# Kernel tuning notes

Measured on AMD Instinct MI355X. Metric: run time of the kernel, lower is better.

Reference implementation:

```python
import jax, jax.numpy as jnp
from jax import lax
import numpy as np

B, S, PRE = 64, 12, 12
N04, N07, N08 = 307, 883, 170
IN_DIM, HID, ENC = 128, 256, 256


def setup_inputs() -> dict:
    key = jax.random.key(0)
    ks = iter(jax.random.split(key, 64))
    nrm = lambda shape, s=1.0: jax.random.normal(next(ks), shape, jnp.float32) * s
    uni = lambda shape: jax.random.uniform(next(ks), shape, jnp.float32)
    d = {
        "vec_pems04": nrm((N04, IN_DIM)),
        "vec_pems07": nrm((N07, IN_DIM)),
        "vec_pems08": nrm((N08, IN_DIM)),
        "feat": nrm((B, S, N04)),
        "adj_pems04": uni((N04, N04)),
        "adj_pems07": uni((N07, N07)),
        "adj_pems08": uni((N08, N08)),
    }
    for p in ("ex4", "ex7", "ex8"):
        d[p + "_W1"] = nrm((IN_DIM, HID), 0.05)
        d[p + "_b1"] = jnp.zeros((HID,), jnp.float32)
        d[p + "_W2"] = nrm((HID, ENC), 0.05)
        d[p + "_b2"] = jnp.zeros((ENC,), jnp.float32)
        d[p + "_g"] = jnp.ones((ENC,), jnp.float32)
        d[p + "_bt"] = jnp.zeros((ENC,), jnp.float32)
        d[p + "_eps"] = jnp.ones((1,), jnp.float32)
    d["gru_W1"] = nrm((HID + 1, 2 * HID), 0.05)
    d["gru_b1"] = jnp.ones((2 * HID,), jnp.float32)  # VGRULinear bias=1.0
    d["gru_W2"] = nrm((HID + 1, HID), 0.05)
    d["gru_b2"] = jnp.zeros((HID,), jnp.float32)
    d["feat_W"] = nrm((ENC, ENC), 0.05)
    d["feat_b"] = jnp.zeros((1,), jnp.float32)
    d["lin_W"] = nrm((HID + ENC, HID), 0.05)
    d["lin_b"] = jnp.zeros((HID,), jnp.float32)
    d["out_W"] = nrm((HID, PRE), 0.05)
    d["out_b"] = jnp.zeros((PRE,), jnp.float32)
    d["eval_flag"] = 0
    return d


def _extract(vec, adj, W1, b1, W2, b2, g, bt, eps1):
    # Extractor_N2V with etype='gin', BatchNorm1d in training mode (batch stats)
    h = vec @ W1 + b1
    pooled = adj @ h
    deg = adj @ jnp.ones((adj.shape[0], 1), adj.dtype)
    h = pooled / deg + eps1 * h
    mu = jnp.mean(h, axis=0)
    var = jnp.mean(jnp.square(h - mu), axis=0)  # biased var, as torch BN
    h = (h - mu) * lax.rsqrt(var + 1e-5) * g + bt
    return h @ W2 + b2


def _predict(feat, node_feat, gru_W1, gru_b1, gru_W2, gru_b2, feat_W, feat_b, lin_W, lin_b):
    Bb, Ss, N = feat.shape
    H = gru_W2.shape[1]
    E = node_feat.shape[-1]
    # feat @ weights + bias is timestep-invariant -> hoist out of the scan (same math)
    fp = jnp.broadcast_to(node_feat[None], (Bb, N, E)).reshape(Bb * N, E) @ feat_W + feat_b

    def vl(x, hs, W, b):
        # VGRULinear: concat scalar input with per-node hidden, flatten per node
        cat = jnp.concatenate([x[..., None], hs.reshape(Bb, N, H)], axis=2).reshape(Bb * N, H + 1)
        return (cat @ W + b).reshape(Bb, -1)

    def step(h, x):
        gates = jax.nn.sigmoid(vl(x, h, gru_W1, gru_b1))  # (B, N*2H)
        r, u = jnp.split(gates, 2, axis=1)                # chunk on flat dim, as in source
        c = jnp.tanh(vl(x, r * h, gru_W2, gru_b2))
        nh = u * h + (1.0 - u) * c
        nh = jnp.concatenate([nh.reshape(Bb * N, H), fp], axis=1) @ lin_W + lin_b
        nh = nh.reshape(Bb, N * H)
        return nh, None

    h0 = jnp.zeros((Bb, N * H), feat.dtype)
    hT, _ = lax.scan(step, h0, jnp.swapaxes(feat, 0, 1))  # scan over seq_len
    return hT.reshape(Bb * N, H)  # last output


def reference(vec_pems04, vec_pems07, vec_pems08, feat, adj_pems04, adj_pems07, adj_pems08,
              ex4_W1, ex4_b1, ex4_W2, ex4_b2, ex4_g, ex4_bt, ex4_eps,
              ex7_W1, ex7_b1, ex7_W2, ex7_b2, ex7_g, ex7_bt, ex7_eps,
              ex8_W1, ex8_b1, ex8_W2, ex8_b2, ex8_g, ex8_bt, ex8_eps,
              gru_W1, gru_b1, gru_W2, gru_b2, feat_W, feat_b, lin_W, lin_b,
              out_W, out_b, eval_flag):
    # dataset='4' != ft_dataset='8', eval=False branch
    f4 = _extract(vec_pems04, adj_pems04, ex4_W1, ex4_b1, ex4_W2, ex4_b2, ex4_g, ex4_bt, ex4_eps)
    f7 = _extract(vec_pems07, adj_pems07, ex7_W1, ex7_b1, ex7_W2, ex7_b2, ex7_g, ex7_bt, ex7_eps)
    f8 = _extract(vec_pems08, adj_pems08, ex8_W1, ex8_b1, ex8_W2, ex8_b2, ex8_g, ex8_bt, ex8_eps)
    last = _predict(feat, f4, gru_W1, gru_b1, gru_W2, gru_b2, feat_W, feat_b, lin_W, lin_b)
    pred = (last @ out_W + out_b).reshape(feat.shape[0], adj_pems04.shape[0], -1)
    return pred, f4, f7, f8
```

## Files before the change

kernel.cpp:

```cpp
#include <hip/hip_runtime.h>
#include <hip/hip_bf16.h>
#include <math.h>

using bf16 = __hip_bfloat16;
using short8  = __attribute__((ext_vector_type(8))) short;
using float4v = __attribute__((ext_vector_type(4))) float;

#define B_   64
#define S_   12
#define N04  307
#define N07  883
#define N08  170
#define BN   (B_ * N04)
#define HID  256
#define ENC  256
#define PRE  12
#define UOFF (N04 * HID)

constexpr int c_Mi[3]   = {N04, N07, N08};
constexpr int c_Kp[3]   = {320, 896, 192};
constexpr int c_Moff[3] = {0, N04, N04 + N07};
constexpr int c_Aoff[3] = {0, N04 * 320, N04 * 320 + N07 * 896};
constexpr int c_Cb[3]   = {0, 320, 320 + 896};
#define MTOT  (N04 + N07 + N08)
#define H0T_LD 1408

#define NT 38
constexpr int g_sz[NT] = {
    39296, 113024, 21760, 235776, 94249, 779689, 28900,
    32768, 256, 65536, 256, 256, 256, 1,
    32768, 256, 65536, 256, 256, 256, 1,
    32768, 256, 65536, 256, 256, 256, 1,
    131584, 512, 65792, 256, 65536, 1, 131072, 256, 3072, 12
};
struct Tables { int off[NT + 1]; int blk[NT + 1]; };
constexpr Tables mk_tables() {
    Tables t{};
    t.off[0] = 0; t.blk[0] = 0;
    for (int i = 0; i < NT; ++i) {
        t.off[i + 1] = t.off[i] + g_sz[i];
        t.blk[i + 1] = t.blk[i] + (g_sz[i] + 1023) / 1024;
    }
    return t;
}
constexpr Tables g_tbl = mk_tables();

static __device__ __forceinline__ float fsigmoid(float t) {
    return __builtin_amdgcn_rcpf(1.f + __expf(-t));
}
static __device__ __forceinline__ float ftanh(float t) {
    return 1.f - 2.f * __builtin_amdgcn_rcpf(__expf(2.f * t) + 1.f);
}

static __device__ __forceinline__ void bsplit(int m, int& b, int& nn) {
    b  = (int)(((unsigned long long)(unsigned)m * 27980243ull) >> 33);
    nn = m - b * N04;
}

__global__ void sniff_kernel(const unsigned short* raw, int* flag)
{
    __shared__ int sh[256];
    int t = threadIdx.x, cnt = 0;
    for (int i = t; i < 2048; i += 256) {
        unsigned int w = ((unsigned int)raw[i]) << 16;
        float a = fabsf(__uint_as_float(w));
        if (a > 1e-3f && a < 100.f) cnt++;
    }
    sh[t] = cnt; __syncthreads();
    for (int off = 128; off > 0; off >>= 1) {
        if (t < off) sh[t] += sh[t + off];
        __syncthreads();
    }
    if (t == 0) *flag = (sh[0] > 1536) ? 1 : 0;
}

struct Ptrs { const void* p[NT]; };

__global__ __launch_bounds__(256) void convert_all(Ptrs a, float* arena, const int* flag)
{
    const int bf = *flag;
    int b = blockIdx.x;
    int t = 0;
    while (b >= g_tbl.blk[t + 1]) ++t;
    const int base = (b - g_tbl.blk[t]) * 1024;
    const int n = g_sz[t];
    const void* src = a.p[t];
    float* dst = arena + g_tbl.off[t];
#pragma unroll
    for (int k = 0; k < 4; ++k) {
        int j = base + k * 256 + threadIdx.x;
        if (j < n)
            dst[j] = bf ? __bfloat162float(((const bf16*)src)[j]) : ((const float*)src)[j];
    }
}

__global__ __launch_bounds__(256) void prep_weights(const float* w1, const float* w2, const float* wl,
                                                    bf16* WgT, bf16* WcT, bf16* WlT)
{
    int id = blockIdx.x * 256 + threadIdx.x;
    if (id < 131072) {
        int n = id >> 8, k = id & 255;
        WgT[id] = __float2bfloat16(w1[(size_t)(1 + k) * 512 + n]);
    } else if (id < 196608) {
        int r = id - 131072; int n = r >> 8, k = r & 255;
        WcT[r] = __float2bfloat16(w2[(size_t)(1 + k) * 256 + n]);
    } else if (id < 262144) {
        int r = id - 196608; int n = r >> 8, k = r & 255;
        WlT[r] = __float2bfloat16(wl[(size_t)k * 256 + n]);
    }
}

__global__ __launch_bounds__(256) void prep_adjB(const float* a4, const float* a7, const float* a8, bf16* adjB)
{
    int z = blockIdx.z;
    int Mi = c_Mi[z], Kp = c_Kp[z];
    int m = blockIdx.x;
    if (m >= Mi) return;
    const float* src = (z == 0) ? a4 : (z == 1) ? a7 : a8;
    bf16* dst = adjB + c_Aoff[z] + (size_t)m * Kp;
    for (int c = threadIdx.x; c < Kp; c += 256)
        dst[c] = (c < Mi) ? __float2bfloat16(src[(size_t)m * Mi + c]) : __float2bfloat16(0.f);
}

__global__ __launch_bounds__(256) void prep_transposes(
    const float* v4, const float* v7, const float* v8,
    const float* w1a, const float* w1b, const float* w1c,
    const float* w2a, const float* w2b, const float* w2c,
    const float* featW, const float* linW, const float* outW,
    bf16* vecB, bf16* W1T, bf16* W2T, bf16* featWT, bf16* linW2T, bf16* outWT)
{
    int id = blockIdx.x * 256 + threadIdx.x;
    if (id < 174080) {
        int r = id >> 7, c = id & 127;
        float v = (r < N04) ? v4[(size_t)r * 128 + c]
                : (r < N04 + N07) ? v7[(size_t)(r - N04) * 128 + c]
                : v8[(size_t)(r - N04 - N07) * 128 + c];
        vecB[id] = __float2bfloat16(v);
    } else if (id < 174080 + 98304) {
        int r = id - 174080; int z = r >> 15; int rem = r & 32767;
        int n = rem >> 7, k = rem & 127;
        const float* w = (z == 0) ? w1a : (z == 1) ? w1b : w1c;
        W1T[r] = __float2bfloat16(w[(size_t)k * 256 + n]);
    } else if (id < 272384 + 196608) {
        int r = id - 272384; int z = r >> 16; int rem = r & 65535;
        int n = rem >> 8, k = rem & 255;
        const float* w = (z == 0) ? w2a : (z == 1) ? w2b : w2c;
        W2T[r] = __float2bfloat16(w[(size_t)k * 256 + n]);
    } else if (id < 468992 + 65536) {
        int r = id - 468992; int n = r >> 8, k = r & 255;
        featWT[r] = __float2bfloat16(featW[(size_t)k * 256 + n]);
    } else if (id < 534528 + 65536) {
        int r = id - 534528; int n = r >> 8, k = r & 255;
        linW2T[r] = __float2bfloat16(linW[(size_t)(256 + k) * 256 + n]);
    } else if (id < 600064 + 16384) {
        int r = id - 600064; int p = r >> 8, k = r & 255;
        outWT[r] = __float2bfloat16((p < PRE) ? outW[(size_t)k * PRE + p] : 0.f);
    }
}
#define PREP_T_TOT (600064 + 16384)

struct GemmZ {
    const unsigned short* A[3];
    const unsigned short* BT[3];
    int M[3]; int K[3]; int lda[3]; int ldb[3];
};

template <typename EP>
__global__ __launch_bounds__(256) void gemm_mfma64(GemmZ p, int Nv, EP ep)
{
    const int z = blockIdx.z;
    const int gx = gridDim.x, gy = gridDim.y;
    const int nwg = gx * gy;
    const int flat = blockIdx.y * gx + blockIdx.x;
    const int xcd = flat & 7, lin = flat >> 3;
    const int q = nwg >> 3, r = nwg & 7;
    const int wg = (xcd < r ? xcd * (q + 1) : r * (q + 1) + (xcd - r) * q) + lin;
    const int bx = wg / gy;
    const int by = wg - bx * gy;

    const int M = p.M[z], K = p.K[z], lda = p.lda[z], ldb = p.ldb[z];
    const int m0 = bx * 64;
    const int n0 = by * 64;
    if (m0 >= M) return;
    __shared__ __align__(16) unsigned short As[64 * 72];
    __shared__ __align__(16) unsigned short Bs[64 * 72];
    const int t = threadIdx.x;
    const int srow  = t >> 2;
    const int skoff = (t & 3) * 16;
    const int lane = t & 63;
    const int w  = t >> 6;
    const int wm = (w & 1) * 32;
    const int wn = (w >> 1) * 32;
    const int l15 = lane & 15;
    const int l4  = lane >> 4;

    float4v acc[2][2];
#pragma unroll
    for (int i = 0; i < 2; ++i)
#pragma unroll
        for (int j = 0; j < 2; ++j) acc[i][j] = (float4v)(0.f);

    const int gm = m0 + srow;
    const bool avalid = (gm < M);
    const unsigned short* aptr = p.A[z]  + (size_t)gm * lda + skoff;
    const unsigned short* bptr = p.BT[z] + (size_t)(n0 + srow) * ldb + skoff;
    unsigned short* asw = &As[srow * 72 + skoff];
    unsigned short* bsw = &Bs[srow * 72 + skoff];
    const uint4 z4 = {0, 0, 0, 0};

    for (int kt = 0; kt < K; kt += 64) {
        uint4 av0 = avalid ? *(const uint4*)(aptr + kt)     : z4;
        uint4 av1 = avalid ? *(const uint4*)(aptr + kt + 8) : z4;
        uint4 bv0 = *(const uint4*)(bptr + kt);
        uint4 bv1 = *(const uint4*)(bptr + kt + 8);
        __syncthreads();
        *(uint4*)(asw)     = av0;
        *(uint4*)(asw + 8) = av1;
        *(uint4*)(bsw)     = bv0;
        *(uint4*)(bsw + 8) = bv1;
        __syncthreads();
#pragma unroll
        for (int ks = 0; ks < 2; ++ks) {
            short8 af[2], bq[2];
#pragma unroll
            for (int mi = 0; mi < 2; ++mi)
                af[mi] = *(const short8*)&As[(wm + mi * 16 + l15) * 72 + ks * 32 + l4 * 8];
#pragma unroll
            for (int ni = 0; ni < 2; ++ni)
                bq[ni] = *(const short8*)&Bs[(wn + ni * 16 + l15) * 72 + ks * 32 + l4 * 8];
#pragma unroll
            for (int mi = 0; mi < 2; ++mi)
#pragma unroll
                for (int ni = 0; ni < 2; ++ni)
                    acc[mi][ni] = __builtin_amdgcn_mfma_f32_16x16x32_bf16(af[mi], bq[ni], acc[mi][ni], 0, 0, 0);
        }
    }
#pragma unroll
    for (int mi = 0; mi < 2; ++mi) {
#pragma unroll
        for (int r2 = 0; r2 < 4; ++r2) {
            int m = m0 + wm + mi * 16 + l4 * 4 + r2;
            if (m >= M) continue;
#pragma unroll
            for (int ni = 0; ni < 2; ++ni) {
                int n = n0 + wn + ni * 16 + l15;
                if (n < Nv) ep(z, m, n, acc[mi][ni][r2]);
            }
        }
    }
}

struct EPg1 {
    const float* b1[3]; float* h0F; bf16* h0T;
    __device__ void operator()(int z, int m, int n, float v) const {
        v += b1[z][n];
        int gr = c_Moff[z] + m;
        h0F[(size_t)gr * 256 + n] = v;
        h0T[(size_t)n * H0T_LD + c_Cb[z] + m] = __float2bfloat16(v);
    }
};
struct EPg2 {
    const float* deg; const float* h0F; float* h1F; const float* eps[3];
    __device__ void operator()(int z, int m, int n, float v) const {
        int gr = c_Moff[z] + m;
        h1F[(size_t)gr * 256 + n] = v / deg[gr] + eps[z][0] * h0F[(size_t)gr * 256 + n];
    }
};
struct EPg3 {
    const float* b2[3]; void* outbase; size_t ooff[3]; const int* flag; bf16* f4B;
    __device__ void operator()(int z, int m, int n, float v) const {
        v += b2[z][n];
        size_t i = ooff[z] + (size_t)m * 256 + n;
        if (*flag) ((bf16*)outbase)[i] = __float2bfloat16(v);
        else       ((float*)outbase)[i] = v;
        if (z == 0) f4B[(size_t)m * 256 + n] = __float2bfloat16(v);
    }
};
struct EPfp2a {
    const float* sb; bf16* fpreB;
    __device__ void operator()(int z, int m, int n, float v) const {
        fpreB[(size_t)m * 256 + n] = __float2bfloat16(v + sb[0]);
    }
};
struct EPfp2b {
    float* fp2;
    __device__ void operator()(int z, int m, int n, float v) const {
        fp2[(size_t)m * 256 + n] = v;
    }
};
struct EPpred {
    const float* ob; void* outbase; const int* flag;
    __device__ void operator()(int z, int m, int n, float v) const {
        v += ob[n];
        size_t i = (size_t)m * PRE + n;
        if (*flag) ((bf16*)outbase)[i] = __float2bfloat16(v);
        else       ((float*)outbase)[i] = v;
    }
};

struct EPgates3 {
    bf16* rh; bf16* ub; const bf16* hB;
    const float* b1; const float* w1r0; const float* feat; int s;
    __device__ void operator()(int z, int m, int n, float v) const {
        int b, nn; bsplit(m, b, nn);
        float x = feat[((size_t)b * S_ + s) * N04 + nn];
        float g = fsigmoid(v + b1[n] + x * w1r0[n]);
        int p = nn * 512 + n;
        int base = b * UOFF;
        if (p < UOFF) {
            int idx = base + p;
            rh[idx] = __float2bfloat16(g * __bfloat162float(hB[idx]));
        } else {
            ub[base + (p - UOFF)] = __float2bfloat16(g);
        }
    }
};
struct EPcand3 {
    bf16* uhc; const bf16* ub; const bf16* hB;
    const float* b2; const float* w2r0; const float* feat; int s;
    __device__ void operator()(int z, int m, int n, float v) const {
        int b, nn; bsplit(m, b, nn);
        float x = feat[((size_t)b * S_ + s) * N04 + nn];
        float c = ftanh(v + b2[n] + x * w2r0[n]);
        size_t idx = (size_t)m * 256 + n;
        float u = __bfloat162float(ub[idx]);
        float h = __bfloat162float(hB[idx]);
        uhc[idx] = __float2bfloat16(u * h + (1.f - u) * c);
    }
};
struct EPlin3 {
    bf16* hB; const float* lb; const float* fp2;
    __device__ void operator()(int z, int m, int n, float v) const {
        int b, nn; bsplit(m, b, nn);
        hB[(size_t)m * 256 + n] = __float2bfloat16(v + lb[n] + fp2[(size_t)nn * 256 + n]);
    }
};

__global__ __launch_bounds__(256) void init_step0(const float* feat,
                                                  const float* b1, const float* w1r0,
                                                  const float* b2, const float* w2r0,
                                                  bf16* uhc)
{
    int m = blockIdx.x, n = threadIdx.x;
    int b, nn; bsplit(m, b, nn);
    const float* fb = feat + (size_t)b * S_ * N04;
    float c = ftanh(b2[n] + fb[nn] * w2r0[n]);
    int p = UOFF + nn * 256 + n;
    int gn = p >> 9, gc = p & 511;
    float u = fsigmoid(b1[gc] + fb[gn] * w1r0[gc]);
    uhc[(size_t)m * 256 + n] = __float2bfloat16((1.f - u) * c);
}

__global__ void deg_all(const float* a4, const float* a7, const float* a8, float* deg)
{
    int z = blockIdx.z;
    int Mi = c_Mi[z];
    int row = blockIdx.x;
    if (row >= Mi) return;
    const float* adj = (z == 0) ? a4 : (z == 1) ? a7 : a8;
    float s = 0.f;
    for (int j = threadIdx.x; j < Mi; j += 64) s += adj[(size_t)row * Mi + j];
#pragma unroll
    for (int off = 32; off > 0; off >>= 1) s += __shfl_down(s, off, 64);
    if (threadIdx.x == 0) deg[c_Moff[z] + row] = s;
}

__global__ __launch_bounds__(256) void stats_all(const float* h1F, float* mu, float* rstd)
{
    int z = blockIdx.z;
    int Mi = c_Mi[z], moff = c_Moff[z];
    int j = blockIdx.x;
    int t = threadIdx.x;
    float s = 0.f, ss = 0.f;
    for (int i = t; i < Mi; i += 256) {
        float v = h1F[(size_t)(moff + i) * 256 + j];
        s += v; ss += v * v;
    }
    __shared__ float sh[256], sh2[256];
    sh[t] = s; sh2[t] = ss;
    __syncthreads();
    for (int off = 128; off > 0; off >>= 1) {
        if (t < off) { sh[t] += sh[t + off]; sh2[t] += sh2[t + off]; }
        __syncthreads();
    }
    if (t == 0) {
        float m = sh[0] / (float)Mi;
        float var = sh2[0] / (float)Mi - m * m;
        mu[z * 256 + j] = m;
        rstd[z * 256 + j] = rsqrtf(var + 1e-5f);
    }
}

__global__ __launch_bounds__(256) void norm_all(const float* h1F, const float* mu, const float* rstd,
                                                const float* ga, const float* gb, const float* gc,
                                                const float* ba, const float* bb, const float* bc,
                                                bf16* nh1B)
{
    int r = blockIdx.x;
    int n = threadIdx.x;
    int z = (r < N04) ? 0 : (r < N04 + N07) ? 1 : 2;
    const float* g  = (z == 0) ? ga : (z == 1) ? gb : gc;
    const float* bt = (z == 0) ? ba : (z == 1) ? bb : bc;
    float v = (h1F[(size_t)r * 256 + n] - mu[z * 256 + n]) * rstd[z * 256 + n] * g[n] + bt[n];
    nh1B[(size_t)r * 256 + n] = __float2bfloat16(v);
}

extern "C" void kernel_launch(void* const* d_in, const int* in_sizes, int n_in,
                              void* d_out, int out_size, void* d_ws, size_t ws_size,
                              hipStream_t stream)
{
    char* wp = (char*)d_ws;
    auto carve = [&](size_t bytes) -> void* {
        void* p = (void*)wp;
        wp += (bytes + 255) & ~(size_t)255;
        return p;
    };
    float* arena = (float*)carve((size_t)g_tbl.off[NT] * 4);
    int*   flag  = (int*)carve(256);
    bf16*  hb_a  = (bf16*)carve((size_t)BN * HID * 2);
    bf16*  hb_b  = (bf16*)carve((size_t)BN * HID * 2);
    bf16*  rh    = (bf16*)carve((size_t)BN * HID * 2);
    bf16*  uhc   = (bf16*)carve((size_t)BN * HID * 2);
    bf16*  ubufB = (bf16*)carve((size_t)BN * HID * 2);
    bf16*  WgT   = (bf16*)carve((size_t)512 * 256 * 2);
    bf16*  WcT   = (bf16*)carve((size_t)256 * 256 * 2);
    bf16*  WlT   = (bf16*)carve((size_t)256 * 256 * 2);
    bf16*  vecB  = (bf16*)carve((size_t)MTOT * 128 * 2);
    bf16*  adjB  = (bf16*)carve((size_t)(N04 * 320 + N07 * 896 + N08 * 192) * 2);
    bf16*  W1T   = (bf16*)carve((size_t)3 * 256 * 128 * 2);
    bf16*  W2T   = (bf16*)carve((size_t)3 * 256 * 256 * 2);
    bf16*  featWT= (bf16*)carve((size_t)256 * 256 * 2);
    bf16*  linW2T= (bf16*)carve((size_t)256 * 256 * 2);
    bf16*  outWT = (bf16*)carve((size_t)64 * 256 * 2);
    float* h0F   = (float*)carve((size_t)MTOT * 256 * 4);
    bf16*  h0T   = (bf16*)carve((size_t)256 * H0T_LD * 2);
    float* h1F   = (float*)carve((size_t)MTOT * 256 * 4);
    bf16*  nh1B  = (bf16*)carve((size_t)MTOT * 256 * 2);
    float* degb  = (float*)carve((size_t)MTOT * 4);
    float* mub   = (float*)carve(3 * 256 * 4);
    float* rstdb = (float*)carve(3 * 256 * 4);
    bf16*  f4B   = (bf16*)carve((size_t)N04 * 256 * 2);
    bf16*  fpreB = (bf16*)carve((size_t)N04 * 256 * 2);
    float* fp2   = (float*)carve((size_t)N04 * 256 * 4);

    sniff_kernel<<<1, 256, 0, stream>>>((const unsigned short*)d_in[0], flag);
    Ptrs ptrs;
    for (int i = 0; i < NT; ++i) ptrs.p[i] = d_in[i];
    convert_all<<<g_tbl.blk[NT], 256, 0, stream>>>(ptrs, arena, flag);

    auto A = [&](int i) -> const float* { return arena + g_tbl.off[i]; };

    prep_weights<<<1024, 256, 0, stream>>>(A(28), A(30), A(34), WgT, WcT, WlT);
    prep_adjB<<<dim3(N07, 1, 3), 256, 0, stream>>>(A(4), A(5), A(6), adjB);
    prep_transposes<<<(PREP_T_TOT + 255) / 256, 256, 0, stream>>>(
        A(0), A(1), A(2), A(7), A(14), A(21), A(9), A(16), A(23),
        A(32), A(34), A(36), vecB, W1T, W2T, featWT, linW2T, outWT);

    hipMemsetAsync(h0T, 0, (size_t)256 * H0T_LD * 2, stream);

    const size_t o_f4 = (size_t)B_ * N04 * PRE;
    const size_t o_f7 = o_f4 + (size_t)N04 * ENC;
    const size_t o_f8 = o_f7 + (size_t)N07 * ENC;

    deg_all<<<dim3(N07, 1, 3), 64, 0, stream>>>(A(4), A(5), A(6), degb);

    {
        GemmZ p;
        for (int z = 0; z < 3; ++z) {
            p.A[z] = (const unsigned short*)(vecB + (size_t)c_Moff[z] * 128);
            p.BT[z] = (const unsigned short*)(W1T + (size_t)z * 256 * 128);
            p.M[z] = c_Mi[z]; p.K[z] = 128; p.lda[z] = 128; p.ldb[z] = 128;
        }
        EPg1 ep{{A(8), A(15), A(22)}, h0F, h0T};
        gemm_mfma64<<<dim3(14, 4, 3), 256, 0, stream>>>(p, 256, ep);
    }
    {
        GemmZ p;
        for (int z = 0; z < 3; ++z) {
            p.A[z] = (const unsigned short*)(adjB + c_Aoff[z]);
            p.BT[z] = (const unsigned short*)(h0T + c_Cb[z]);
            p.M[z] = c_Mi[z]; p.K[z] = c_Kp[z]; p.lda[z] = c_Kp[z]; p.ldb[z] = H0T_LD;
        }
        EPg2 ep{degb, h0F, h1F, {A(13), A(20), A(27)}};
        gemm_mfma64<<<dim3(14, 4, 3), 256, 0, stream>>>(p, 256, ep);
    }
    stats_all<<<dim3(256, 1, 3), 256, 0, stream>>>(h1F, mub, rstdb);
    norm_all<<<MTOT, 256, 0, stream>>>(h1F, mub, rstdb, A(11), A(18), A(25), A(12), A(19), A(26), nh1B);
    {
        GemmZ p;
        for (int z = 0; z < 3; ++z) {
            p.A[z] = (const unsigned short*)(nh1B + (size_t)c_Moff[z] * 256);
            p.BT[z] = (const unsigned short*)(W2T + (size_t)z * 256 * 256);
            p.M[z] = c_Mi[z]; p.K[z] = 256; p.lda[z] = 256; p.ldb[z] = 256;
        }
        EPg3 ep{{A(10), A(17), A(24)}, d_out, {o_f4, o_f7, o_f8}, flag, f4B};
        gemm_mfma64<<<dim3(14, 4, 3), 256, 0, stream>>>(p, 256, ep);
    }
    {
        GemmZ p{};
        p.A[0] = (const unsigned short*)f4B; p.BT[0] = (const unsigned short*)featWT;
        p.M[0] = N04; p.K[0] = 256; p.lda[0] = 256; p.ldb[0] = 256;
        gemm_mfma64<<<dim3(5, 4, 1), 256, 0, stream>>>(p, 256, EPfp2a{A(33), fpreB});
        p.A[0] = (const unsigned short*)fpreB; p.BT[0] = (const unsigned short*)linW2T;
        gemm_mfma64<<<dim3(5, 4, 1), 256, 0, stream>>>(p, 256, EPfp2b{fp2});
    }

    const float* feat = A(3);
    bf16* hcB = hb_a;
    bf16* hnB = hb_b;
    for (int s = 0; s < S_; ++s) {
        GemmZ p{};
        p.M[0] = BN; p.K[0] = 256; p.lda[0] = 256; p.ldb[0] = 256;
        if (s == 0) {
            init_step0<<<BN, 256, 0, stream>>>(feat, A(29), A(28), A(31), A(30), uhc);
        } else {
            p.A[0] = (const unsigned short*)hcB; p.BT[0] = (const unsigned short*)WgT;
            gemm_mfma64<<<dim3(BN / 64, 8, 1), 256, 0, stream>>>(p, 512,
                EPgates3{rh, ubufB, hcB, A(29), A(28), feat, s});
            p.A[0] = (const unsigned short*)rh; p.BT[0] = (const unsigned short*)WcT;
            gemm_mfma64<<<dim3(BN / 64, 4, 1), 256, 0, stream>>>(p, 256,
                EPcand3{uhc, ubufB, hcB, A(31), A(30), feat, s});
        }
        p.A[0] = (const unsigned short*)uhc; p.BT[0] = (const unsigned short*)WlT;
        gemm_mfma64<<<dim3(BN / 64, 4, 1), 256, 0, stream>>>(p, 256,
            EPlin3{hnB, A(35), fp2});
        bf16* tb = hcB; hcB = hnB; hnB = tb;
    }

    {
        GemmZ p{};
        p.A[0] = (const unsigned short*)hcB; p.BT[0] = (const unsigned short*)outWT;
        p.M[0] = BN; p.K[0] = 256; p.lda[0] = 256; p.ldb[0] = 256;
        gemm_mfma64<<<dim3(BN / 64, 1, 1), 256, 0, stream>>>(p, PRE, EPpred{A(37), d_out, flag});
    }
}
```

Before: 791.5 us.

## Pre-pack recurrent weights into MFMA fragment order and read B directly from global

The recurrent GRU/linear/output weights are now repacked at prep time so that each 16x32 MFMA B-fragment is contiguous per lane. A new specialized GEMM kernel (fixed K=256, no M bounds check, occupancy hint of 4) stages only A through shared memory and loads B fragments straight from global/L2. This is meant to remove B tile staging and its LDS traffic and barriers in the per-step GEMMs, at the cost of relying on cache hits for repeated B reads and on BN being a multiple of 64.

```diff
diff --git a/kernel.cpp b/kernel.cpp
--- a/kernel.cpp
+++ b/kernel.cpp
@@ -95,18 +95,29 @@
 }
 
 __global__ __launch_bounds__(256) void prep_weights(const float* w1, const float* w2, const float* wl,
-                                                    bf16* WgT, bf16* WcT, bf16* WlT)
+                                                    bf16* WgP, bf16* WcP, bf16* WlP)
 {
     int id = blockIdx.x * 256 + threadIdx.x;
     if (id < 131072) {
-        int n = id >> 8, k = id & 255;
-        WgT[id] = __float2bfloat16(w1[(size_t)(1 + k) * 512 + n]);
+        int tile = id >> 9, within = id & 511;
+        int lane = within >> 3, e = within & 7;
+        int n = (tile >> 3) * 16 + (lane & 15);
+        int k = (tile & 7) * 32 + (lane >> 4) * 8 + e;
+        WgP[id] = __float2bfloat16(w1[(size_t)(1 + k) * 512 + n]);
     } else if (id < 196608) {
-        int r = id - 131072; int n = r >> 8, k = r & 255;
-        WcT[r] = __float2bfloat16(w2[(size_t)(1 + k) * 256 + n]);
+        int r = id - 131072;
+        int tile = r >> 9, within = r & 511;
+        int lane = within >> 3, e = within & 7;
+        int n = (tile >> 3) * 16 + (lane & 15);
+        int k = (tile & 7) * 32 + (lane >> 4) * 8 + e;
+        WcP[r] = __float2bfloat16(w2[(size_t)(1 + k) * 256 + n]);
     } else if (id < 262144) {
-        int r = id - 196608; int n = r >> 8, k = r & 255;
-        WlT[r] = __float2bfloat16(wl[(size_t)k * 256 + n]);
+        int r = id - 196608;
+        int tile = r >> 9, within = r & 511;
+        int lane = within >> 3, e = within & 7;
+        int n = (tile >> 3) * 16 + (lane & 15);
+        int k = (tile & 7) * 32 + (lane >> 4) * 8 + e;
+        WlP[r] = __float2bfloat16(wl[(size_t)k * 256 + n]);
     }
 }
 
@@ -127,7 +138,7 @@
     const float* w1a, const float* w1b, const float* w1c,
     const float* w2a, const float* w2b, const float* w2c,
     const float* featW, const float* linW, const float* outW,
-    bf16* vecB, bf16* W1T, bf16* W2T, bf16* featWT, bf16* linW2T, bf16* outWT)
+    bf16* vecB, bf16* W1T, bf16* W2T, bf16* featWT, bf16* linW2T, bf16* outWP)
 {
     int id = blockIdx.x * 256 + threadIdx.x;
     if (id < 174080) {
@@ -153,8 +164,12 @@
         int r = id - 534528; int n = r >> 8, k = r & 255;
         linW2T[r] = __float2bfloat16(linW[(size_t)(256 + k) * 256 + n]);
     } else if (id < 600064 + 16384) {
-        int r = id - 600064; int p = r >> 8, k = r & 255;
-        outWT[r] = __float2bfloat16((p < PRE) ? outW[(size_t)k * PRE + p] : 0.f);
+        int r = id - 600064;
+        int tile = r >> 9, within = r & 511;
+        int lane = within >> 3, e = within & 7;
+        int p = (tile >> 3) * 16 + (lane & 15);
+        int k = (tile & 7) * 32 + (lane >> 4) * 8 + e;
+        outWP[r] = __float2bfloat16((p < PRE) ? outW[(size_t)k * PRE + p] : 0.f);
     }
 }
 #define PREP_T_TOT (600064 + 16384)
@@ -250,6 +265,81 @@
     }
 }
 
+struct GemmB { const unsigned short* A; const unsigned short* Bp; int M; };
+
+template <typename EP>
+__global__ __launch_bounds__(256, 4) void gemm_bd(GemmB p, int Nv, EP ep)
+{
+    const int gx = gridDim.x, gy = gridDim.y;
+    const int nwg = gx * gy;
+    const int flat = blockIdx.y * gx + blockIdx.x;
+    const int xcd = flat & 7, lin = flat >> 3;
+    const int q = nwg >> 3, r = nwg & 7;
+    const int wg = (xcd < r ? xcd * (q + 1) : r * (q + 1) + (xcd - r) * q) + lin;
+    const int bx = wg / gy;
+    const int by = wg - bx * gy;
+    const int m0 = bx * 64;
+    const int n0 = by * 64;
+
+    __shared__ __align__(16) unsigned short As[64 * 72];
+    const int t = threadIdx.x;
+    const int srow  = t >> 2;
+    const int skoff = (t & 3) * 16;
+    const int lane = t & 63;
+    const int w  = t >> 6;
+    const int wm = (w & 1) * 32;
+    const int wn = (w >> 1) * 32;
+    const int l15 = lane & 15;
+    const int l4  = lane >> 4;
+
+    float4v acc[2][2];
+#pragma unroll
+    for (int i = 0; i < 2; ++i)
+#pragma unroll
+        for (int j = 0; j < 2; ++j) acc[i][j] = (float4v)(0.f);
+
+    const unsigned short* aptr = p.A + (size_t)(m0 + srow) * 256 + skoff;
+    unsigned short* asw = &As[srow * 72 + skoff];
+    const unsigned short* bbase = p.Bp + (((size_t)((n0 + wn) >> 4) * 8) << 9) + (lane << 3);
+
+#pragma unroll
+    for (int kt = 0; kt < 4; ++kt) {
+        uint4 av0 = *(const uint4*)(aptr + kt * 64);
+        uint4 av1 = *(const uint4*)(aptr + kt * 64 + 8);
+        __syncthreads();
+        *(uint4*)(asw)     = av0;
+        *(uint4*)(asw + 8) = av1;
+        __syncthreads();
+#pragma unroll
+        for (int ks = 0; ks < 2; ++ks) {
+            const int kc = kt * 2 + ks;
+            short8 af[2], bq[2];
+#pragma unroll
+            for (int mi = 0; mi < 2; ++mi)
+                af[mi] = *(const short8*)&As[(wm + mi * 16 + l15) * 72 + ks * 32 + l4 * 8];
+            bq[0] = *(const short8*)(bbase + ((size_t)kc << 9));
+            bq[1] = *(const short8*)(bbase + ((size_t)(kc + 8) << 9));
+#pragma unroll
+            for (int mi = 0; mi < 2; ++mi)
+#pragma unroll
+                for (int ni = 0; ni < 2; ++ni)
+                    acc[mi][ni] = __builtin_amdgcn_mfma_f32_16x16x32_bf16(af[mi], bq[ni], acc[mi][ni], 0, 0, 0);
+        }
+    }
+#pragma unroll
+    for (int mi = 0; mi < 2; ++mi) {
+#pragma unroll
+        for (int r2 = 0; r2 < 4; ++r2) {
+            const int m = m0 + wm + mi * 16 + l4 * 4 + r2;
+#pragma unroll
+            for (int ni = 0; ni < 2; ++ni) {
+                const int n = n0 + wn + ni * 16 + l15;
+                if (n < Nv) ep(0, m, n, acc[mi][ni][r2]);
+            }
+        }
+    }
+}
+
 struct EPg1 {
     const float* b1[3]; float* h0F; bf16* h0T;
     __device__ void operator()(int z, int m, int n, float v) const {
@@ -422,16 +512,16 @@
     bf16*  rh    = (bf16*)carve((size_t)BN * HID * 2);
     bf16*  uhc   = (bf16*)carve((size_t)BN * HID * 2);
     bf16*  ubufB = (bf16*)carve((size_t)BN * HID * 2);
-    bf16*  WgT   = (bf16*)carve((size_t)512 * 256 * 2);
-    bf16*  WcT   = (bf16*)carve((size_t)256 * 256 * 2);
-    bf16*  WlT   = (bf16*)carve((size_t)256 * 256 * 2);
+    bf16*  WgP   = (bf16*)carve((size_t)512 * 256 * 2);
+    bf16*  WcP   = (bf16*)carve((size_t)256 * 256 * 2);
+    bf16*  WlP   = (bf16*)carve((size_t)256 * 256 * 2);
     bf16*  vecB  = (bf16*)carve((size_t)MTOT * 128 * 2);
     bf16*  adjB  = (bf16*)carve((size_t)(N04 * 320 + N07 * 896 + N08 * 192) * 2);
     bf16*  W1T   = (bf16*)carve((size_t)3 * 256 * 128 * 2);
     bf16*  W2T   = (bf16*)carve((size_t)3 * 256 * 256 * 2);
     bf16*  featWT= (bf16*)carve((size_t)256 * 256 * 2);
     bf16*  linW2T= (bf16*)carve((size_t)256 * 256 * 2);
-    bf16*  outWT = (bf16*)carve((size_t)64 * 256 * 2);
+    bf16*  outWP = (bf16*)carve((size_t)64 * 256 * 2);
     float* h0F   = (float*)carve((size_t)MTOT * 256 * 4);
     bf16*  h0T   = (bf16*)carve((size_t)256 * H0T_LD * 2);
     float* h1F   = (float*)carve((size_t)MTOT * 256 * 4);
@@ -450,11 +540,11 @@
 
     auto A = [&](int i) -> const float* { return arena + g_tbl.off[i]; };
 
-    prep_weights<<<1024, 256, 0, stream>>>(A(28), A(30), A(34), WgT, WcT, WlT);
+    prep_weights<<<1024, 256, 0, stream>>>(A(28), A(30), A(34), WgP, WcP, WlP);
     prep_adjB<<<dim3(N07, 1, 3), 256, 0, stream>>>(A(4), A(5), A(6), adjB);
     prep_transposes<<<(PREP_T_TOT + 255) / 256, 256, 0, stream>>>(
         A(0), A(1), A(2), A(7), A(14), A(21), A(9), A(16), A(23),
-        A(32), A(34), A(36), vecB, W1T, W2T, featWT, linW2T, outWT);
+        A(32), A(34), A(36), vecB, W1T, W2T, featWT, linW2T, outWP);
 
     hipMemsetAsync(h0T, 0, (size_t)256 * H0T_LD * 2, stream);
 
@@ -509,28 +599,24 @@
     bf16* hcB = hb_a;
     bf16* hnB = hb_b;
     for (int s = 0; s < S_; ++s) {
-        GemmZ p{};
-        p.M[0] = BN; p.K[0] = 256; p.lda[0] = 256; p.ldb[0] = 256;
         if (s == 0) {
             init_step0<<<BN, 256, 0, stream>>>(feat, A(29), A(28), A(31), A(30), uhc);
         } else {
-            p.A[0] = (const unsigned short*)hcB; p.BT[0] = (const unsigned short*)WgT;
-            gemm_mfma64<<<dim3(BN / 64, 8, 1), 256, 0, stream>>>(p, 512,
+            GemmB pg{(const unsigned short*)hcB, (const unsigned short*)WgP, BN};
+            gemm_bd<<<dim3(BN / 64, 8, 1), 256, 0, stream>>>(pg, 512,
                 EPgates3{rh, ubufB, hcB, A(29), A(28), feat, s});
-            p.A[0] = (const unsigned short*)rh; p.BT[0] = (const unsigned short*)WcT;
-            gemm_mfma64<<<dim3(BN / 64, 4, 1), 256, 0, stream>>>(p, 256,
+            GemmB pc{(const unsigned short*)rh, (const unsigned short*)WcP, BN};
+            gemm_bd<<<dim3(BN / 64, 4, 1), 256, 0, stream>>>(pc, 256,
                 EPcand3{uhc, ubufB, hcB, A(31), A(30), feat, s});
         }
-        p.A[0] = (const unsigned short*)uhc; p.BT[0] = (const unsigned short*)WlT;
-        gemm_mfma64<<<dim3(BN / 64, 4, 1), 256, 0, stream>>>(p, 256,
+        GemmB pl{(const unsigned short*)uhc, (const unsigned short*)WlP, BN};
+        gemm_bd<<<dim3(BN / 64, 4, 1), 256, 0, stream>>>(pl, 256,
             EPlin3{hnB, A(35), fp2});
         bf16* tb = hcB; hcB = hnB; hnB = tb;
     }
 
     {
-        GemmZ p{};
-        p.A[0] = (const unsigned short*)hcB; p.BT[0] = (const unsigned short*)outWT;
-        p.M[0] = BN; p.K[0] = 256; p.lda[0] = 256; p.ldb[0] = 256;
-        gemm_mfma64<<<dim3(BN / 64, 1, 1), 256, 0, stream>>>(p, PRE, EPpred{A(37), d_out, flag});
-    }
-}
+        GemmB pp{(const unsigned short*)hcB, (const unsigned short*)outWP, BN};
+        gemm_bd<<<dim3(BN / 64, 1, 1), 256, 0, stream>>>(pp, PRE, EPpred{A(37), d_out, flag});
+    }
+}
```

After: 743.8 us. -6.0%, faster.
